# Kernel optimization log

Measured on AMD Instinct MI355X. Metric: run time of the kernel, lower is better.

The kernel has to match this reference:

```python
import jax, jax.numpy as jnp
import numpy as np

D_MODEL, N_HEADS, D_HEAD = 1024, 16, 64
BATCH, SEQ = 4, 2048


def setup_inputs() -> dict:
    key = jax.random.key(0)
    ks = jax.random.split(key, 10)
    s = 1.0 / np.sqrt(D_MODEL)
    x = jax.random.normal(ks[0], (BATCH, SEQ, D_MODEL), dtype=jnp.float32)
    attention_mask = jax.random.randint(ks[1], (BATCH, SEQ), 0, 2).astype(jnp.bool_)
    # guarantee at least one attended key per batch row (avoid all -inf softmax)
    attention_mask = attention_mask.at[:, 0].set(True)
    def lin(k):
        kw, kb = jax.random.split(k)
        W = jax.random.uniform(kw, (D_MODEL, D_MODEL), jnp.float32, -s, s)
        b = jax.random.uniform(kb, (D_MODEL,), jnp.float32, -s, s)
        return W, b
    Wq, bq = lin(ks[2]); Wk, bk = lin(ks[3]); Wv, bv = lin(ks[4]); Wo, bo = lin(ks[5])
    return {"x": x, "attention_mask": attention_mask,
            "Wq": Wq, "bq": bq, "Wk": Wk, "bk": bk,
            "Wv": Wv, "bv": bv, "Wo": Wo, "bo": bo}


def reference(x, attention_mask, Wq, bq, Wk, bk, Wv, bv, Wo, bo):
    B, S, _ = x.shape
    def proj(W, b):  # [B,S,d_model] -> [B,S,H,Dh]
        return (x @ W + b).reshape(B, S, N_HEADS, D_HEAD)
    q = proj(Wq, bq)
    k = proj(Wk, bk)
    v = proj(Wv, bv)
    scores = jnp.einsum('bqhd,bkhd->bhqk', q, k)  # [B,H,S,S]
    add_mask = jnp.where(attention_mask, 0.0, jnp.inf)[:, None, None, :]
    # faithful order: subtract mask, THEN scale (inf survives division)
    probs = jax.nn.softmax((scores - add_mask) / jnp.sqrt(jnp.float32(D_HEAD)), axis=-1)
    attn = jnp.einsum('bhqk,bkhd->bqhd', probs, v).reshape(B, S, N_HEADS * D_HEAD)
    return attn @ Wo + bo
```

## Files before the change

### kernel.cpp

```cpp
#include <hip/hip_runtime.h>
#include <hip/hip_bf16.h>
#include <math.h>

#define BATCH 4
#define SEQ   2048
#define DM    1024
#define NH    16
#define DH    64
#define MROWS (BATCH * SEQ)

typedef unsigned short ushort_t;
typedef unsigned int   uint_t;
typedef __attribute__((ext_vector_type(8))) short  short8;
typedef __attribute__((ext_vector_type(4))) float  float4v;

#define QSCALE 0.1803368801111244f

__device__ __forceinline__ ushort_t f2bf(float v) {
    uint_t u = __float_as_uint(v);
    u += 0x7FFFu + ((u >> 16) & 1u);
    return (ushort_t)(u >> 16);
}
__device__ __forceinline__ float bf2f(ushort_t h) {
    return __uint_as_float(((uint_t)h) << 16);
}
__device__ __forceinline__ void gload_lds16(const ushort_t* g, ushort_t* lds) {
    __builtin_amdgcn_global_load_lds(
        (const __attribute__((address_space(1))) void*)g,
        (__attribute__((address_space(3))) void*)lds, 16, 0, 0);
}

__global__ __launch_bounds__(256) void conv_x(
    const float* __restrict__ src, ushort_t* __restrict__ dst, int n4)
{
    int i = blockIdx.x * 256 + threadIdx.x;
    if (i >= n4) return;
    float4 v = ((const float4*)src)[i];
    ((ushort4*)dst)[i] = make_ushort4(f2bf(v.x), f2bf(v.y), f2bf(v.z), f2bf(v.w));
}

__global__ __launch_bounds__(256) void convT_w4(
    const float* __restrict__ W0, const float* __restrict__ W1,
    const float* __restrict__ W2, const float* __restrict__ W3,
    ushort_t* __restrict__ fused, ushort_t* __restrict__ woh,
    ushort_t* __restrict__ wol)
{
    __shared__ float sT[64][65];
    const int z = blockIdx.z;
    const float* W = (z == 0) ? W0 : (z == 1) ? W1 : (z == 2) ? W2 : W3;
    ushort_t* ht = (z < 3) ? fused + (size_t)z * 1024 * 1024 : woh;
    const int n0 = blockIdx.x * 64, k0 = blockIdx.y * 64;
    const int t = threadIdx.x;
#pragma unroll
    for (int i = 0; i < 16; i++) {
        int idx = t + i * 256, r = idx >> 6, c = idx & 63;
        sT[r][c] = W[(size_t)(k0 + r) * 1024 + n0 + c];
    }
    __syncthreads();
#pragma unroll
    for (int i = 0; i < 16; i++) {
        int idx = t + i * 256, r = idx >> 6, c = idx & 63;
        float v = sT[c][r];
        ushort_t h = f2bf(v);
        ht[(size_t)(n0 + r) * 1024 + k0 + c] = h;
        if (z == 3) wol[(size_t)(n0 + r) * 1024 + k0 + c] = f2bf(v - bf2f(h));
    }
}

#define BAR()   asm volatile("s_barrier" ::: "memory")
#define LGKM0() asm volatile("s_waitcnt lgkmcnt(0)" ::: "memory")
#define VMW6()  asm volatile("s_waitcnt vmcnt(6)" ::: "memory")

#define STAGE_A(BO, KT) do {                                                 \
    const ushort_t* _s = prowA + (size_t)((KT) & 15) * 64;                   \
    gload_lds16(_s,         &smem[(BO) + dstw]);                             \
    gload_lds16(_s + 65536, &smem[(BO) + 4096 + dstw]);                      \
  } while (0)

#define STAGE_B(BO, KT) do {                                                 \
    const ushort_t* _s = prowB + (size_t)((KT) & 15) * 64;                   \
    gload_lds16(_s,          &smem[(BO) + 8192  + dstw]);                    \
    gload_lds16(_s + 65536,  &smem[(BO) + 12288 + dstw]);                    \
    gload_lds16(_s + 131072, &smem[(BO) + 16384 + dstw]);                    \
    gload_lds16(_s + 196608, &smem[(BO) + 20480 + dstw]);                    \
  } while (0)

#define LOAD_AV(BO) do {                                                     \
    _Pragma("unroll")                                                        \
    for (int mf = 0; mf < 4; mf++) {                                         \
      av[mf][0] = *(const short8*)&smem[(BO) + aAm + mf * 1024 + aA0];       \
      av[mf][1] = *(const short8*)&smem[(BO) + aAm + mf * 1024 + aA1];       \
    }                                                                        \
  } while (0)

#define LOAD_BV(BO, NQ) do {                                                 \
    _Pragma("unroll")                                                        \
    for (int nf = 0; nf < 2; nf++) {                                         \
      bvf[nf][0] = *(const short8*)&smem[(BO) + 8192 + aBn + (NQ) * 2048 +   \
                                         nf * 1024 + aA0];                   \
      bvf[nf][1] = *(const short8*)&smem[(BO) + 8192 + aBn + (NQ) * 2048 +   \
                                         nf * 1024 + aA1];                   \
    }                                                                        \
  } while (0)

#define MFMA_H(NQ) do {                                                      \
    __builtin_amdgcn_s_setprio(1);                                           \
    _Pragma("unroll")                                                        \
    for (int kk = 0; kk < 2; kk++)                                           \
      _Pragma("unroll")                                                      \
      for (int nf = 0; nf < 2; nf++)                                         \
        _Pragma("unroll")                                                    \
        for (int mf = 0; mf < 4; mf++)                                       \
          acc[mf][(NQ) * 2 + nf] =                                           \
              __builtin_amdgcn_mfma_f32_16x16x32_bf16(                       \
                  av[mf][kk], bvf[nf][kk], acc[mf][(NQ) * 2 + nf], 0, 0, 0); \
    __builtin_amdgcn_s_setprio(0);                                           \
  } while (0)

__global__ __launch_bounds__(512, 2) void gemm_qkv(
    const ushort_t* __restrict__ A, const ushort_t* __restrict__ Bt,
    const float* __restrict__ bq, const float* __restrict__ bk,
    const float* __restrict__ bv, const int* __restrict__ mask,
    ushort_t* __restrict__ Qh, ushort_t* __restrict__ Kh,
    ushort_t* __restrict__ Vt)
{
    __shared__ __align__(16) ushort_t smem[73728];
    const int t = threadIdx.x, lane = t & 63, w = t >> 6;

    int bid = blockIdx.y * 12 + blockIdx.x;
    bid = (bid & 7) * 96 + (bid >> 3);
    const int n0 = (bid % 12) * 256, m0 = (bid / 12) * 128;

    const int wm = w >> 2, wn = w & 3;
    const int lq = lane >> 4, lc = lane & 15;
    const int gl = (lane & 7) ^ ((lane >> 3) & 7);
    const int sect = n0 >> 10;
    const float* bsel = (sect == 0) ? bq : (sect == 1) ? bk : bv;
    const float scl = (sect == 0) ? QSCALE : 1.0f;

    const ushort_t* prowA = A  + (size_t)(m0 + w * 8 + (lane >> 3)) * 1024 + gl * 8;
    const ushort_t* prowB = Bt + (size_t)(n0 + w * 8 + (lane >> 3)) * 1024 + gl * 8;
    const int dstw = w * 512;

    const int aA0 = lc * 64 + ((lq ^ (lc & 7)) * 8);
    const int aA1 = lc * 64 + (((4 + lq) ^ (lc & 7)) * 8);
    const int aAm = wm * 4096;
    const int aBn = wn * 4096;

    float4v acc[4][4];
#pragma unroll
    for (int i = 0; i < 4; i++)
#pragma unroll
        for (int j = 0; j < 4; j++) acc[i][j] = (float4v)(0.0f);

    short8 av[4][2], bvf[2][2];

    STAGE_A(0, 0); STAGE_B(0, 0); STAGE_A(24576, 1); STAGE_B(24576, 1);
    VMW6();
    BAR();

    int bc = 0, bs = 49152;
    for (int kt = 0; kt < 16; kt++) {
        LOAD_AV(bc); LOAD_BV(bc, 0); STAGE_A(bs, kt + 2);
        BAR(); LGKM0(); MFMA_H(0); BAR();
        LOAD_BV(bc, 1); STAGE_B(bs, kt + 2);
        BAR(); LGKM0(); MFMA_H(1); VMW6(); BAR();
        bc = (bc == 49152) ? 0 : bc + 24576;
        bs = (bs == 49152) ? 0 : bs + 24576;
    }

#pragma unroll
    for (int nf = 0; nf < 4; nf++) {
        const int nn = (n0 + wn * 64 + nf * 16 + lc) & 1023;
        const float bvv = bsel[nn];
        const int h = nn >> 6, d = nn & 63;
#pragma unroll
        for (int mf = 0; mf < 4; mf++) {
            const int mbase = m0 + wm * 64 + mf * 16 + lq * 4;
            const int b = mbase >> 11, s0 = mbase & 2047;
            int mk[4] = {1, 1, 1, 1};
            if (sect != 0) {
                const int4 m4 = *(const int4*)&mask[b * 2048 + s0];
                mk[0] = m4.x; mk[1] = m4.y; mk[2] = m4.z; mk[3] = m4.w;
            }
            if (sect == 2) {
                ushort_t hh[4];
#pragma unroll
                for (int r = 0; r < 4; r++)
                    hh[r] = mk[r] ? f2bf(acc[mf][nf][r] + bvv) : (ushort_t)0;
                *(ushort4*)&Vt[((size_t)(b * 16 + h) * 64 + d) * 2048 + s0] =
                    make_ushort4(hh[0], hh[1], hh[2], hh[3]);
            } else {
                ushort_t* dst = (sect == 0) ? Qh : Kh;
#pragma unroll
                for (int r = 0; r < 4; r++)
                    dst[((size_t)(b * 16 + h) * 2048 + s0 + r) * 64 + d] =
                        mk[r] ? f2bf((acc[mf][nf][r] + bvv) * scl) : (ushort_t)0;
            }
        }
    }
}

#undef STAGE_A
#undef STAGE_B
#undef LOAD_AV
#undef LOAD_BV
#undef MFMA_H

__global__ __launch_bounds__(256) void gemm_split3(
    const ushort_t* __restrict__ Ah, const ushort_t* __restrict__ Al,
    const ushort_t* __restrict__ Bh, const ushort_t* __restrict__ Bl,
    const float* __restrict__ bias, float* __restrict__ out)
{
    __shared__ __align__(16) ushort_t smem[16384];
    const int t = threadIdx.x, lane = t & 63, w = t >> 6;
    const int n0 = blockIdx.x * 128, m0 = blockIdx.y * 128;
    const int wm = (w >> 1) * 64, wn = (w & 1) * 64;
    const int lq = lane >> 4, lc = lane & 15;
    const int gl = (lane & 3) ^ ((lane >> 3) & 3);
    const int irow = lane >> 2;

    float4v acc[4][4];
#pragma unroll
    for (int i = 0; i < 4; i++)
#pragma unroll
        for (int j = 0; j < 4; j++) acc[i][j] = (float4v)(0.0f);

    const ushort_t* plane = (w == 0) ? Ah : (w == 1) ? Al : (w == 2) ? Bh : Bl;
    const size_t prow = (size_t)(((w < 2) ? m0 : n0) + irow) * 1024 + gl * 8;

    for (int k0 = 0; k0 < 1024; k0 += 32) {
        __syncthreads();
#pragma unroll
        for (int j = 0; j < 8; j++)
            gload_lds16(plane + prow + (size_t)j * 16384 + k0, &smem[w * 4096 + j * 512]);
        __syncthreads();

        short8 ah[4], al[4];
#pragma unroll
        for (int mt = 0; mt < 4; mt++) {
            const int r = wm + mt * 16 + lc;
            const int off = r * 32 + ((lq ^ ((r >> 1) & 3)) * 8);
            ah[mt] = *(const short8*)&smem[off];
            al[mt] = *(const short8*)&smem[4096 + off];
        }
#pragma unroll
        for (int nt = 0; nt < 4; nt++) {
            const int r = wn + nt * 16 + lc;
            const int off = r * 32 + ((lq ^ ((r >> 1) & 3)) * 8);
            short8 bh = *(const short8*)&smem[8192 + off];
            short8 bl = *(const short8*)&smem[12288 + off];
#pragma unroll
            for (int mt = 0; mt < 4; mt++) {
                acc[mt][nt] = __builtin_amdgcn_mfma_f32_16x16x32_bf16(ah[mt], bh, acc[mt][nt], 0, 0, 0);
                acc[mt][nt] = __builtin_amdgcn_mfma_f32_16x16x32_bf16(al[mt], bh, acc[mt][nt], 0, 0, 0);
                acc[mt][nt] = __builtin_amdgcn_mfma_f32_16x16x32_bf16(ah[mt], bl, acc[mt][nt], 0, 0, 0);
            }
        }
    }

#pragma unroll
    for (int nt = 0; nt < 4; nt++) {
        const int n = n0 + wn + nt * 16 + lc;
        const float bvv = bias[n];
#pragma unroll
        for (int mt = 0; mt < 4; mt++)
#pragma unroll
            for (int r = 0; r < 4; r++) {
                const int m = m0 + wm + mt * 16 + lq * 4 + r;
                out[(size_t)m * 1024 + n] = acc[mt][nt][r] + bvv;
            }
    }
}

__global__ __launch_bounds__(512, 4) void flash_mfma(
    const ushort_t* __restrict__ Q, const ushort_t* __restrict__ K,
    const ushort_t* __restrict__ Vt, const int* __restrict__ mask,
    ushort_t* __restrict__ Oh, ushort_t* __restrict__ Ol)
{
    __shared__ __align__(16) ushort_t smem[32768];
    const int t = threadIdx.x, lane = t & 63, w = t >> 6;
    const int q0 = blockIdx.x * 256;
    const int bh = blockIdx.y, b = bh >> 4, h = bh & 15;
    const int lq = lane >> 4, lc = lane & 15;
    const int wm = w * 32;
    const int gl = (lane & 7) ^ ((lane >> 3) & 7);
    const int lc7 = lc & 7;

    const short8 onesf = (short8)(lc == 0 ? (short)0x3F80 : (short)0);

    {
        const int4 a = ((const int4*)(mask + b * SEQ))[t];
        int cnt = (a.x == 0) + (a.y == 0) + (a.z == 0) + (a.w == 0);
#pragma unroll
        for (int off = 1; off < 64; off <<= 1) cnt += __shfl_xor(cnt, off);
        if (lane == 0) ((float*)&smem[28672])[w] = (float)cnt;
    }
#pragma unroll
    for (int j = 0; j < 4; j++) {
        const int i = w * 4 + j;
        gload_lds16(Q + ((size_t)bh * SEQ + q0 + i * 8 + (lane >> 3)) * 64 + gl * 8,
                    &smem[i * 512]);
    }
    const ushort_t* gsrc;
    int gstride, jstride, dstb;
    if (w < 4) {
        gsrc = K + ((size_t)bh * SEQ + w * 16 + (lane >> 3)) * 64 + gl * 8;
        gstride = 64 * 64;  jstride = 8 * 64;   dstb = 16384 + w * 1024;
    } else {
        gsrc = Vt + ((size_t)bh * 64 + (w - 4) * 16 + (lane >> 3)) * SEQ + gl * 8;
        gstride = 64;       jstride = 8 * SEQ;  dstb = 24576 + (w - 4) * 1024;
    }
    gload_lds16(gsrc,           &smem[dstb]);
    gload_lds16(gsrc + jstride, &smem[dstb + 512]);
    gsrc += gstride;

    __syncthreads();

    const float* cs = (const float*)&smem[28672];
    const float nmaskf = cs[0] + cs[1] + cs[2] + cs[3] +
                         cs[4] + cs[5] + cs[6] + cs[7];

    short8 aq[2][2];
#pragma unroll
    for (int mt = 0; mt < 2; mt++)
#pragma unroll
        for (int kk = 0; kk < 2; kk++) {
            const int r = wm + mt * 16 + lc;
            aq[mt][kk] = *(const short8*)&smem[r * 64 + (((kk * 4 + lq) ^ (r & 7)) * 8)];
        }

    int aK[2], aPw[4], aPr[2];
#pragma unroll
    for (int kk = 0; kk < 2; kk++) {
        aK[kk]  = lc * 64 + (((kk * 4 + lq) ^ lc7) * 8);
        aPr[kk] = wm * 64 + aK[kk];
    }
#pragma unroll
    for (int kt4 = 0; kt4 < 4; kt4++)
        aPw[kt4] = wm * 64 + lc * 64 + (((kt4 * 2 + (lq >> 1)) ^ lc7) * 8) + (lq & 1) * 4;

    float4v O[2][4];
    float4v lacc[2];
#pragma unroll
    for (int mt = 0; mt < 2; mt++) {
#pragma unroll
        for (int nt = 0; nt < 4; nt++) O[mt][nt] = (float4v)(0.0f);
        lacc[mt] = (float4v)(0.0f);
    }

    __syncthreads();

    for (int kt = 0; kt < 32; kt++) {
        const int cur = (kt & 1) * 4096;
        const int nxt = cur ^ 4096;

        if (kt < 31) {
            gload_lds16(gsrc,           &smem[dstb + nxt]);
            gload_lds16(gsrc + jstride, &smem[dstb + nxt + 512]);
            gsrc += gstride;
        }

#pragma unroll
        for (int kt4 = 0; kt4 < 4; kt4++) {
            float4v s0 = (float4v)(0.0f), s1 = (float4v)(0.0f);
#pragma unroll
            for (int kk = 0; kk < 2; kk++) {
                short8 ak = *(const short8*)&smem[16384 + cur + kt4 * 1024 + aK[kk]];
                s0 = __builtin_amdgcn_mfma_f32_16x16x32_bf16(ak, aq[0][kk], s0, 0, 0, 0);
                s1 = __builtin_amdgcn_mfma_f32_16x16x32_bf16(ak, aq[1][kk], s1, 0, 0, 0);
            }
            {
                const float p0 = __builtin_amdgcn_exp2f(s0[0]);
                const float p1 = __builtin_amdgcn_exp2f(s0[1]);
                const float p2 = __builtin_amdgcn_exp2f(s0[2]);
                const float p3 = __builtin_amdgcn_exp2f(s0[3]);
                __hip_bfloat162 pk01 = __float22bfloat162_rn(make_float2(p0, p1));
                __hip_bfloat162 pk23 = __float22bfloat162_rn(make_float2(p2, p3));
                *(uint2*)&smem[aPw[kt4]] =
                    make_uint2(*(const uint_t*)&pk01, *(const uint_t*)&pk23);
            }
            {
                const float p0 = __builtin_amdgcn_exp2f(s1[0]);
                const float p1 = __builtin_amdgcn_exp2f(s1[1]);
                const float p2 = __builtin_amdgcn_exp2f(s1[2]);
                const float p3 = __builtin_amdgcn_exp2f(s1[3]);
                __hip_bfloat162 pk01 = __float22bfloat162_rn(make_float2(p0, p1));
                __hip_bfloat162 pk23 = __float22bfloat162_rn(make_float2(p2, p3));
                *(uint2*)&smem[1024 + aPw[kt4]] =
                    make_uint2(*(const uint_t*)&pk01, *(const uint_t*)&pk23);
            }
        }

#pragma unroll
        for (int kk = 0; kk < 2; kk++) {
            short8 ap[2];
#pragma unroll
            for (int mt = 0; mt < 2; mt++)
                ap[mt] = *(const short8*)&smem[mt * 1024 + aPr[kk]];
            __builtin_amdgcn_s_setprio(1);
#pragma unroll
            for (int mt = 0; mt < 2; mt++)
                lacc[mt] = __builtin_amdgcn_mfma_f32_16x16x32_bf16(ap[mt], onesf, lacc[mt], 0, 0, 0);
#pragma unroll
            for (int nt = 0; nt < 4; nt++) {
                short8 bv = *(const short8*)&smem[24576 + cur + nt * 1024 + aK[kk]];
#pragma unroll
                for (int mt = 0; mt < 2; mt++)
                    O[mt][nt] = __builtin_amdgcn_mfma_f32_16x16x32_bf16(ap[mt], bv, O[mt][nt], 0, 0, 0);
            }
            __builtin_amdgcn_s_setprio(0);
        }

        asm volatile("s_waitcnt vmcnt(0)" ::: "memory");
        asm volatile("s_barrier" ::: "memory");
    }

#pragma unroll
    for (int mt = 0; mt < 2; mt++) {
#pragma unroll
        for (int r = 0; r < 4; r++) {
            const float lsum = __shfl(lacc[mt][r], lane & 48) - nmaskf;
            const float inv = 1.0f / lsum;
            const int srow = q0 + wm + mt * 16 + lq * 4 + r;
#pragma unroll
            for (int nt = 0; nt < 4; nt++) {
                const float v = O[mt][nt][r] * inv;
                const ushort_t hh = f2bf(v);
                const size_t idx = ((size_t)(b * SEQ + srow)) * 1024 + h * 64 + nt * 16 + lc;
                Oh[idx] = hh;
                Ol[idx] = f2bf(v - bf2f(hh));
            }
        }
    }
}

#undef BAR
#undef LGKM0
#undef VMW6

extern "C" void kernel_launch(void* const* d_in, const int* in_sizes, int n_in,
                              void* d_out, int out_size, void* d_ws, size_t ws_size,
                              hipStream_t stream) {
    const float* x    = (const float*)d_in[0];
    const int*   mask = (const int*)d_in[1];
    const float* Wq   = (const float*)d_in[2];
    const float* bq   = (const float*)d_in[3];
    const float* Wk   = (const float*)d_in[4];
    const float* bk   = (const float*)d_in[5];
    const float* Wv   = (const float*)d_in[6];
    const float* bv   = (const float*)d_in[7];
    const float* Wo   = (const float*)d_in[8];
    const float* bo   = (const float*)d_in[9];
    float* out = (float*)d_out;

    ushort_t* p = (ushort_t*)d_ws;
    const size_t PLANE  = (size_t)MROWS * DM;
    const size_t WPLANE = (size_t)DM * DM;
    ushort_t* xh  = p;  p += PLANE;
    ushort_t* wf  = p;  p += 3 * WPLANE;
    ushort_t* woh = p;  p += WPLANE;
    ushort_t* wol = p;  p += WPLANE;
    ushort_t* Qh  = p;  p += PLANE;
    ushort_t* Kh  = p;  p += PLANE;
    ushort_t* Vth = p;  p += PLANE;
    ushort_t* Ath = p;  p += PLANE;
    ushort_t* Atl = p;  p += PLANE;

    dim3 blk(256);
    hipLaunchKernelGGL(conv_x, dim3(8192), blk, 0, stream, x, xh, 2097152);
    hipLaunchKernelGGL(convT_w4, dim3(16, 16, 4), blk, 0, stream,
                       Wq, Wk, Wv, Wo, wf, woh, wol);
    hipLaunchKernelGGL(gemm_qkv, dim3(12, 64), dim3(512), 0, stream,
                       xh, wf, bq, bk, bv, mask, Qh, Kh, Vth);
    hipLaunchKernelGGL(flash_mfma, dim3(8, 64), dim3(512), 0, stream,
                       Qh, Kh, Vth, mask, Ath, Atl);
    hipLaunchKernelGGL(gemm_split3, dim3(8, 64), blk, 0, stream,
                       Ath, Atl, woh, wol, bo, out);
}
```

Before: 311.8 us.

## Replace QKV GEMM 128x256 triple-buffered tile with 128x128 double-buffered tile

The QKV projection GEMM moves from 512-thread blocks computing 128x256 tiles with BK=64 and three LDS buffers to 256-thread blocks computing 128x128 tiles with BK=32 and two LDS buffers. LDS drops from 144KB to 32KB per block, which allows more resident blocks per CU and a simpler loop with one barrier per K step. The cost is less operand reuse per tile, more K iterations and barriers, and a full vmcnt(0) wait each step that removes the deeper prefetch.

Result: no change. 316.6 us (+1.6%).

```diff
diff --git a/kernel.cpp b/kernel.cpp
--- a/kernel.cpp
+++ b/kernel.cpp
@@ -67,85 +67,36 @@
     }
 }
 
-#define BAR()   asm volatile("s_barrier" ::: "memory")
-#define LGKM0() asm volatile("s_waitcnt lgkmcnt(0)" ::: "memory")
-#define VMW6()  asm volatile("s_waitcnt vmcnt(6)" ::: "memory")
-
-#define STAGE_A(BO, KT) do {                                                 \
-    const ushort_t* _s = prowA + (size_t)((KT) & 15) * 64;                   \
-    gload_lds16(_s,         &smem[(BO) + dstw]);                             \
-    gload_lds16(_s + 65536, &smem[(BO) + 4096 + dstw]);                      \
-  } while (0)
-
-#define STAGE_B(BO, KT) do {                                                 \
-    const ushort_t* _s = prowB + (size_t)((KT) & 15) * 64;                   \
-    gload_lds16(_s,          &smem[(BO) + 8192  + dstw]);                    \
-    gload_lds16(_s + 65536,  &smem[(BO) + 12288 + dstw]);                    \
-    gload_lds16(_s + 131072, &smem[(BO) + 16384 + dstw]);                    \
-    gload_lds16(_s + 196608, &smem[(BO) + 20480 + dstw]);                    \
-  } while (0)
-
-#define LOAD_AV(BO) do {                                                     \
-    _Pragma("unroll")                                                        \
-    for (int mf = 0; mf < 4; mf++) {                                         \
-      av[mf][0] = *(const short8*)&smem[(BO) + aAm + mf * 1024 + aA0];       \
-      av[mf][1] = *(const short8*)&smem[(BO) + aAm + mf * 1024 + aA1];       \
-    }                                                                        \
-  } while (0)
-
-#define LOAD_BV(BO, NQ) do {                                                 \
-    _Pragma("unroll")                                                        \
-    for (int nf = 0; nf < 2; nf++) {                                         \
-      bvf[nf][0] = *(const short8*)&smem[(BO) + 8192 + aBn + (NQ) * 2048 +   \
-                                         nf * 1024 + aA0];                   \
-      bvf[nf][1] = *(const short8*)&smem[(BO) + 8192 + aBn + (NQ) * 2048 +   \
-                                         nf * 1024 + aA1];                   \
-    }                                                                        \
-  } while (0)
-
-#define MFMA_H(NQ) do {                                                      \
-    __builtin_amdgcn_s_setprio(1);                                           \
-    _Pragma("unroll")                                                        \
-    for (int kk = 0; kk < 2; kk++)                                           \
-      _Pragma("unroll")                                                      \
-      for (int nf = 0; nf < 2; nf++)                                         \
-        _Pragma("unroll")                                                    \
-        for (int mf = 0; mf < 4; mf++)                                       \
-          acc[mf][(NQ) * 2 + nf] =                                           \
-              __builtin_amdgcn_mfma_f32_16x16x32_bf16(                       \
-                  av[mf][kk], bvf[nf][kk], acc[mf][(NQ) * 2 + nf], 0, 0, 0); \
-    __builtin_amdgcn_s_setprio(0);                                           \
-  } while (0)
-
-__global__ __launch_bounds__(512, 2) void gemm_qkv(
+__global__ __launch_bounds__(256, 4) void gemm_qkv(
     const ushort_t* __restrict__ A, const ushort_t* __restrict__ Bt,
     const float* __restrict__ bq, const float* __restrict__ bk,
     const float* __restrict__ bv, const int* __restrict__ mask,
     ushort_t* __restrict__ Qh, ushort_t* __restrict__ Kh,
     ushort_t* __restrict__ Vt)
 {
-    __shared__ __align__(16) ushort_t smem[73728];
+    __shared__ __align__(16) ushort_t smem[16384];
     const int t = threadIdx.x, lane = t & 63, w = t >> 6;
 
-    int bid = blockIdx.y * 12 + blockIdx.x;
-    bid = (bid & 7) * 96 + (bid >> 3);
-    const int n0 = (bid % 12) * 256, m0 = (bid / 12) * 128;
-
-    const int wm = w >> 2, wn = w & 3;
+    int bid = blockIdx.y * 24 + blockIdx.x;
+    bid = (bid & 7) * 192 + (bid >> 3);
+    const int n0 = (bid % 24) * 128, m0 = (bid / 24) * 128;
+
+    const int wm = (w >> 1) * 64, wn = (w & 1) * 64;
     const int lq = lane >> 4, lc = lane & 15;
-    const int gl = (lane & 7) ^ ((lane >> 3) & 7);
     const int sect = n0 >> 10;
     const float* bsel = (sect == 0) ? bq : (sect == 1) ? bk : bv;
     const float scl = (sect == 0) ? QSCALE : 1.0f;
 
-    const ushort_t* prowA = A  + (size_t)(m0 + w * 8 + (lane >> 3)) * 1024 + gl * 8;
-    const ushort_t* prowB = Bt + (size_t)(n0 + w * 8 + (lane >> 3)) * 1024 + gl * 8;
-    const int dstw = w * 512;
-
-    const int aA0 = lc * 64 + ((lq ^ (lc & 7)) * 8);
-    const int aA1 = lc * 64 + (((4 + lq) ^ (lc & 7)) * 8);
-    const int aAm = wm * 4096;
-    const int aBn = wn * 4096;
+    const int sA = t >> 3;
+    const int cA = (t & 7) ^ (sA & 7);
+    const int r0 = 2 * sA + (cA >> 2);
+    const ushort_t* pA = A  + (size_t)(m0 + r0) * 1024 + (cA & 3) * 8;
+    const ushort_t* pB = Bt + (size_t)(n0 + r0) * 1024 + (cA & 3) * 8;
+    const int toff = t * 8;
+
+    const int aA = (lc >> 1) * 64 + ((((lc & 1) * 4 + lq) ^ (lc >> 1)) * 8);
+    const int aAm = (w >> 1) * 2048;
+    const int aBn = (w & 1) * 2048;
 
     float4v acc[4][4];
 #pragma unroll
@@ -153,30 +104,55 @@
 #pragma unroll
         for (int j = 0; j < 4; j++) acc[i][j] = (float4v)(0.0f);
 
-    short8 av[4][2], bvf[2][2];
-
-    STAGE_A(0, 0); STAGE_B(0, 0); STAGE_A(24576, 1); STAGE_B(24576, 1);
-    VMW6();
-    BAR();
-
-    int bc = 0, bs = 49152;
-    for (int kt = 0; kt < 16; kt++) {
-        LOAD_AV(bc); LOAD_BV(bc, 0); STAGE_A(bs, kt + 2);
-        BAR(); LGKM0(); MFMA_H(0); BAR();
-        LOAD_BV(bc, 1); STAGE_B(bs, kt + 2);
-        BAR(); LGKM0(); MFMA_H(1); VMW6(); BAR();
-        bc = (bc == 49152) ? 0 : bc + 24576;
-        bs = (bs == 49152) ? 0 : bs + 24576;
+    gload_lds16(pA,         &smem[toff]);
+    gload_lds16(pA + 65536, &smem[2048 + toff]);
+    gload_lds16(pB,         &smem[4096 + toff]);
+    gload_lds16(pB + 65536, &smem[6144 + toff]);
+    asm volatile("s_waitcnt vmcnt(0)" ::: "memory");
+    asm volatile("s_barrier" ::: "memory");
+
+    for (int kt = 0; kt < 32; kt++) {
+        const int cur = (kt & 1) * 8192;
+        const int nxt = cur ^ 8192;
+
+        if (kt < 31) {
+            const ushort_t* nA = pA + (kt + 1) * 32;
+            const ushort_t* nB = pB + (kt + 1) * 32;
+            gload_lds16(nA,         &smem[nxt + toff]);
+            gload_lds16(nA + 65536, &smem[nxt + 2048 + toff]);
+            gload_lds16(nB,         &smem[nxt + 4096 + toff]);
+            gload_lds16(nB + 65536, &smem[nxt + 6144 + toff]);
+        }
+
+        short8 av[4], bv[4];
+#pragma unroll
+        for (int mf = 0; mf < 4; mf++)
+            av[mf] = *(const short8*)&smem[cur + aAm + mf * 512 + aA];
+#pragma unroll
+        for (int nf = 0; nf < 4; nf++)
+            bv[nf] = *(const short8*)&smem[cur + 4096 + aBn + nf * 512 + aA];
+
+        __builtin_amdgcn_s_setprio(1);
+#pragma unroll
+        for (int nf = 0; nf < 4; nf++)
+#pragma unroll
+            for (int mf = 0; mf < 4; mf++)
+                acc[mf][nf] = __builtin_amdgcn_mfma_f32_16x16x32_bf16(
+                    av[mf], bv[nf], acc[mf][nf], 0, 0, 0);
+        __builtin_amdgcn_s_setprio(0);
+
+        asm volatile("s_waitcnt vmcnt(0)" ::: "memory");
+        asm volatile("s_barrier" ::: "memory");
     }
 
 #pragma unroll
     for (int nf = 0; nf < 4; nf++) {
-        const int nn = (n0 + wn * 64 + nf * 16 + lc) & 1023;
+        const int nn = (n0 + wn + nf * 16 + lc) & 1023;
         const float bvv = bsel[nn];
         const int h = nn >> 6, d = nn & 63;
 #pragma unroll
         for (int mf = 0; mf < 4; mf++) {
-            const int mbase = m0 + wm * 64 + mf * 16 + lq * 4;
+            const int mbase = m0 + wm + mf * 16 + lq * 4;
             const int b = mbase >> 11, s0 = mbase & 2047;
             int mk[4] = {1, 1, 1, 1};
             if (sect != 0) {
@@ -200,12 +176,6 @@
         }
     }
 }
-
-#undef STAGE_A
-#undef STAGE_B
-#undef LOAD_AV
-#undef LOAD_BV
-#undef MFMA_H
 
 __global__ __launch_bounds__(256) void gemm_split3(
     const ushort_t* __restrict__ Ah, const ushort_t* __restrict__ Al,
@@ -434,10 +404,6 @@
         }
     }
 }
-
-#undef BAR
-#undef LGKM0
-#undef VMW6
 
 extern "C" void kernel_launch(void* const* d_in, const int* in_sizes, int n_in,
                               void* d_out, int out_size, void* d_ws, size_t ws_size,
@@ -471,7 +437,7 @@
     hipLaunchKernelGGL(conv_x, dim3(8192), blk, 0, stream, x, xh, 2097152);
     hipLaunchKernelGGL(convT_w4, dim3(16, 16, 4), blk, 0, stream,
                        Wq, Wk, Wv, Wo, wf, woh, wol);
-    hipLaunchKernelGGL(gemm_qkv, dim3(12, 64), dim3(512), 0, stream,
+    hipLaunchKernelGGL(gemm_qkv, dim3(24, 64), blk, 0, stream,
                        xh, wf, bq, bk, bv, mask, Qh, Kh, Vth);
     hipLaunchKernelGGL(flash_mfma, dim3(8, 64), dim3(512), 0, stream,
                        Qh, Kh, Vth, mask, Ath, Atl);
```

## Pipeline output-projection split-bf16 GEMM with triple-buffered LDS and larger tiles

Applied to the files above, without the earlier changes.

Rewrites the final output-projection GEMM (three-term split-bf16 MFMA) to use 512 threads on 128x256 tiles with a three-stage LDS ring buffer. Global-to-LDS loads for step k+2 are issued while MFMAs for step k run, and MFMA bursts get raised wave priority. Block IDs are remapped for better L2 locality. The cost is much more LDS per block (144 KB), which limits occupancy, plus more complex barrier logic that moves the BAR/LGKM0/VMW6 macros earlier in the file.

Result: no change. 311.4 us (-0.1%).

```diff
diff --git a/kernel.cpp b/kernel.cpp
--- a/kernel.cpp
+++ b/kernel.cpp
@@ -207,18 +207,62 @@
 #undef LOAD_BV
 #undef MFMA_H
 
-__global__ __launch_bounds__(256) void gemm_split3(
+#define S3_STAGE3A(BO, KT) do {                                              \
+    const size_t _k = (size_t)((KT) & 31) * 32;                              \
+    gload_lds16(pAh + _k, &smem[(BO) + toff]);                               \
+    gload_lds16(pAl + _k, &smem[(BO) + 4096 + toff]);                        \
+    gload_lds16(pBh + _k, &smem[(BO) + 8192 + toff]);                        \
+  } while (0)
+
+#define S3_STAGE3B(BO, KT) do {                                              \
+    const size_t _k = (size_t)((KT) & 31) * 32;                              \
+    gload_lds16(pBh + 131072 + _k, &smem[(BO) + 12288 + toff]);              \
+    gload_lds16(pBl + _k,          &smem[(BO) + 16384 + toff]);              \
+    gload_lds16(pBl + 131072 + _k, &smem[(BO) + 20480 + toff]);              \
+  } while (0)
+
+#define S3_MFMA(NQ) do {                                                     \
+    __builtin_amdgcn_s_setprio(1);                                           \
+    _Pragma("unroll")                                                        \
+    for (int nf = 0; nf < 2; nf++)                                           \
+      _Pragma("unroll")                                                      \
+      for (int mf = 0; mf < 4; mf++) {                                       \
+        float4v* _a = &acc[mf][(NQ) * 2 + nf];                               \
+        *_a = __builtin_amdgcn_mfma_f32_16x16x32_bf16(ah[mf], bh[nf], *_a, 0, 0, 0); \
+        *_a = __builtin_amdgcn_mfma_f32_16x16x32_bf16(al[mf], bh[nf], *_a, 0, 0, 0); \
+        *_a = __builtin_amdgcn_mfma_f32_16x16x32_bf16(ah[mf], bl[nf], *_a, 0, 0, 0); \
+      }                                                                      \
+    __builtin_amdgcn_s_setprio(0);                                           \
+  } while (0)
+
+__global__ __launch_bounds__(512, 2) void gemm_split3(
     const ushort_t* __restrict__ Ah, const ushort_t* __restrict__ Al,
     const ushort_t* __restrict__ Bh, const ushort_t* __restrict__ Bl,
     const float* __restrict__ bias, float* __restrict__ out)
 {
-    __shared__ __align__(16) ushort_t smem[16384];
+    __shared__ __align__(16) ushort_t smem[73728];
     const int t = threadIdx.x, lane = t & 63, w = t >> 6;
-    const int n0 = blockIdx.x * 128, m0 = blockIdx.y * 128;
-    const int wm = (w >> 1) * 64, wn = (w & 1) * 64;
+
+    int bid = blockIdx.y * 4 + blockIdx.x;
+    bid = (bid & 7) * 32 + (bid >> 3);
+    const int n0 = (bid % 4) * 256, m0 = (bid / 4) * 128;
+
+    const int wm = w >> 2, wn = w & 3;
     const int lq = lane >> 4, lc = lane & 15;
-    const int gl = (lane & 3) ^ ((lane >> 3) & 3);
-    const int irow = lane >> 2;
+
+    const int prow = t >> 2;
+    const int pc = (t & 3) ^ (prow & 3);
+    const size_t offA = (size_t)(m0 + prow) * 1024 + pc * 8;
+    const size_t offB = (size_t)(n0 + prow) * 1024 + pc * 8;
+    const ushort_t* pAh = Ah + offA;
+    const ushort_t* pAl = Al + offA;
+    const ushort_t* pBh = Bh + offB;
+    const ushort_t* pBl = Bl + offB;
+    const int toff = t * 8;
+
+    const int aR = lc * 32 + ((lq ^ (lc & 3)) * 8);
+    const int aAm = wm * 2048;
+    const int aBn = wn * 2048;
 
     float4v acc[4][4];
 #pragma unroll
@@ -226,52 +270,60 @@
 #pragma unroll
         for (int j = 0; j < 4; j++) acc[i][j] = (float4v)(0.0f);
 
-    const ushort_t* plane = (w == 0) ? Ah : (w == 1) ? Al : (w == 2) ? Bh : Bl;
-    const size_t prow = (size_t)(((w < 2) ? m0 : n0) + irow) * 1024 + gl * 8;
-
-    for (int k0 = 0; k0 < 1024; k0 += 32) {
-        __syncthreads();
-#pragma unroll
-        for (int j = 0; j < 8; j++)
-            gload_lds16(plane + prow + (size_t)j * 16384 + k0, &smem[w * 4096 + j * 512]);
-        __syncthreads();
-
-        short8 ah[4], al[4];
-#pragma unroll
-        for (int mt = 0; mt < 4; mt++) {
-            const int r = wm + mt * 16 + lc;
-            const int off = r * 32 + ((lq ^ ((r >> 1) & 3)) * 8);
-            ah[mt] = *(const short8*)&smem[off];
-            al[mt] = *(const short8*)&smem[4096 + off];
-        }
-#pragma unroll
-        for (int nt = 0; nt < 4; nt++) {
-            const int r = wn + nt * 16 + lc;
-            const int off = r * 32 + ((lq ^ ((r >> 1) & 3)) * 8);
-            short8 bh = *(const short8*)&smem[8192 + off];
-            short8 bl = *(const short8*)&smem[12288 + off];
-#pragma unroll
-            for (int mt = 0; mt < 4; mt++) {
-                acc[mt][nt] = __builtin_amdgcn_mfma_f32_16x16x32_bf16(ah[mt], bh, acc[mt][nt], 0, 0, 0);
-                acc[mt][nt] = __builtin_amdgcn_mfma_f32_16x16x32_bf16(al[mt], bh, acc[mt][nt], 0, 0, 0);
-                acc[mt][nt] = __builtin_amdgcn_mfma_f32_16x16x32_bf16(ah[mt], bl, acc[mt][nt], 0, 0, 0);
-            }
-        }
-    }
-
-#pragma unroll
-    for (int nt = 0; nt < 4; nt++) {
-        const int n = n0 + wn + nt * 16 + lc;
+    short8 ah[4], al[4], bh[2], bl[2];
+
+    S3_STAGE3A(0, 0);     S3_STAGE3B(0, 0);
+    S3_STAGE3A(24576, 1); S3_STAGE3B(24576, 1);
+    VMW6();
+    BAR();
+
+    int bc = 0, bs = 49152;
+    for (int kt = 0; kt < 32; kt++) {
+#pragma unroll
+        for (int mf = 0; mf < 4; mf++) {
+            ah[mf] = *(const short8*)&smem[bc + aAm + mf * 512 + aR];
+            al[mf] = *(const short8*)&smem[bc + 4096 + aAm + mf * 512 + aR];
+        }
+#pragma unroll
+        for (int nf = 0; nf < 2; nf++) {
+            bh[nf] = *(const short8*)&smem[bc + 8192 + aBn + nf * 512 + aR];
+            bl[nf] = *(const short8*)&smem[bc + 16384 + aBn + nf * 512 + aR];
+        }
+        S3_STAGE3A(bs, kt + 2);
+        BAR(); LGKM0(); S3_MFMA(0); BAR();
+
+#pragma unroll
+        for (int nf = 0; nf < 2; nf++) {
+            bh[nf] = *(const short8*)&smem[bc + 8192 + aBn + 1024 + nf * 512 + aR];
+            bl[nf] = *(const short8*)&smem[bc + 16384 + aBn + 1024 + nf * 512 + aR];
+        }
+        S3_STAGE3B(bs, kt + 2);
+        BAR(); LGKM0(); S3_MFMA(1); VMW6(); BAR();
+
+        bc = (bc == 49152) ? 0 : bc + 24576;
+        bs = (bs == 49152) ? 0 : bs + 24576;
+    }
+
+#pragma unroll
+    for (int nf = 0; nf < 4; nf++) {
+        const int n = n0 + wn * 64 + nf * 16 + lc;
         const float bvv = bias[n];
 #pragma unroll
-        for (int mt = 0; mt < 4; mt++)
+        for (int mf = 0; mf < 4; mf++)
 #pragma unroll
             for (int r = 0; r < 4; r++) {
-                const int m = m0 + wm + mt * 16 + lq * 4 + r;
-                out[(size_t)m * 1024 + n] = acc[mt][nt][r] + bvv;
-            }
-    }
-}
+                const int m = m0 + wm * 64 + mf * 16 + lq * 4 + r;
+                out[(size_t)m * 1024 + n] = acc[mf][nf][r] + bvv;
+            }
+    }
+}
+
+#undef S3_STAGE3A
+#undef S3_STAGE3B
+#undef S3_MFMA
+#undef BAR
+#undef LGKM0
+#undef VMW6
 
 __global__ __launch_bounds__(512, 4) void flash_mfma(
     const ushort_t* __restrict__ Q, const ushort_t* __restrict__ K,
@@ -434,10 +486,6 @@
         }
     }
 }
-
-#undef BAR
-#undef LGKM0
-#undef VMW6
 
 extern "C" void kernel_launch(void* const* d_in, const int* in_sizes, int n_in,
                               void* d_out, int out_size, void* d_ws, size_t ws_size,
@@ -475,6 +523,6 @@
                        xh, wf, bq, bk, bv, mask, Qh, Kh, Vth);
     hipLaunchKernelGGL(flash_mfma, dim3(8, 64), dim3(512), 0, stream,
                        Qh, Kh, Vth, mask, Ath, Atl);
-    hipLaunchKernelGGL(gemm_split3, dim3(8, 64), blk, 0, stream,
+    hipLaunchKernelGGL(gemm_split3, dim3(4, 64), dim3(512), 0, stream,
                        Ath, Atl, woh, wol, bo, out);
 }
```
